# Performance work log

Hardware: AMD Instinct MI355X
Metric: run time of the kernel (lower is better)

Reference implementation:

```python
import jax, jax.numpy as jnp
import numpy as np

B, H, L, D, S = 4, 16, 4096, 64, 128

def setup_inputs() -> dict:
    key = jax.random.key(0)
    k1, k2 = jax.random.split(key)
    x = jax.random.normal(k1, (B, H, L, D), dtype=jnp.float32)
    c = jax.random.normal(k2, (H, S, D), dtype=jnp.float32)
    # codebook rows are unit-normalized at init (matches torch init)
    c = c / jnp.linalg.norm(c, axis=-1, keepdims=True)
    return {"x": x, "c": c}

def reference(x, c):
    # cosine-similarity scores: [B,H,L,S]
    cos_sim = jnp.einsum('bhld,hsd->bhls', x, c)
    delta_index = jnp.argmax(cos_sim, axis=-1)            # [B,H,L]
    delta_onehot = jax.nn.one_hot(delta_index, c.shape[-2], dtype=jnp.float32)  # [B,H,L,S]
    return (delta_onehot, c)
```

## Files before the change

### kernel.cpp

```cpp
#include <hip/hip_runtime.h>
#include <math.h>

constexpr int BB = 4;
constexpr int HH = 16;
constexpr int LL = 4096;
constexpr int DD = 64;
constexpr int SS = 128;
constexpr int BM = 128;

constexpr float TAU = 2e-3f;

typedef __attribute__((ext_vector_type(8))) short bf16x8;
typedef __attribute__((ext_vector_type(4))) float f32x4;

#define MFMA16 __builtin_amdgcn_mfma_f32_16x16x32_bf16

__device__ __forceinline__ unsigned short f2bf(float v) {
    unsigned u = __float_as_uint(v);
    return (unsigned short)((u + 0x7fffu + ((u >> 16) & 1u)) >> 16);
}

__device__ __forceinline__ void split8(const float4 va, const float4 vb,
                                       uint4* hi, uint4* lo) {
    const float v[8] = {va.x, va.y, va.z, va.w, vb.x, vb.y, vb.z, vb.w};
    unsigned hw[4], lw[4];
    #pragma unroll
    for (int p = 0; p < 4; ++p) {
        const unsigned u0 = __float_as_uint(v[2 * p]);
        const unsigned u1 = __float_as_uint(v[2 * p + 1]);
        const unsigned h0 = u0 & 0xffff0000u;
        const unsigned h1 = u1 & 0xffff0000u;
        hw[p] = (u0 >> 16) | h1;
        lw[p] = (unsigned)f2bf(v[2 * p] - __uint_as_float(h0))
              | ((unsigned)f2bf(v[2 * p + 1] - __uint_as_float(h1)) << 16);
    }
    *hi = make_uint4(hw[0], hw[1], hw[2], hw[3]);
    *lo = make_uint4(lw[0], lw[1], lw[2], lw[3]);
}

union FragU { uint4 q; bf16x8 v; };

__global__ __launch_bounds__(256) void convert_c_kernel(
    const float* __restrict__ c, unsigned char* __restrict__ ws)
{
    const int sid = blockIdx.x * 256 + threadIdx.x;
    const int h  = sid >> 10;
    const int r  = sid & 1023;
    const int kt = r >> 9;
    const int ct = (r >> 6) & 7;
    const int ln = r & 63;
    const int cc = ct * 16 + (ln & 15);
    const int k0 = kt * 32 + (ln >> 4) * 8;
    const float4* src = (const float4*)(c + ((size_t)h * SS + cc) * DD + k0);
    uint4 hi, lo;
    split8(src[0], src[1], &hi, &lo);
    unsigned char* base =
        ws + (size_t)h * 32768 + (size_t)(((kt << 3) | ct) * 1024 + ln * 16);
    *(uint4*)(base) = hi;
    *(uint4*)(base + 16384) = lo;
}

template <bool USE_WS>
__global__ __launch_bounds__(256) void quantizer_kernel(
    const float* __restrict__ x,
    const float* __restrict__ c,
    const unsigned char* __restrict__ ws,
    float* __restrict__ out,
    float* __restrict__ out_c)
{
    __shared__ __align__(16) unsigned char smemB[32768];
    __shared__ int amax[BM];
    __shared__ int s_nflag;
    __shared__ int s_flag[BM];
    __shared__ float s_fsc[SS];

    const int tid = threadIdx.x;
    const int wv = tid >> 6;
    const int lane = tid & 63;
    const int ln15 = lane & 15;
    const int blk = blockIdx.x;
    const long long r0 = (long long)blk * BM;
    const int h = (int)((r0 >> 12) & (HH - 1));
    const float* __restrict__ chead = c + (size_t)h * SS * DD;

    if (tid == 0) s_nflag = 0;

    if (USE_WS) {
        const unsigned char* wsb = ws + (size_t)h * 32768;
        #pragma unroll
        for (int it = 0; it < 8; ++it) {
            const unsigned off = (unsigned)(wv * 8192 + it * 1024);
            __builtin_amdgcn_global_load_lds(
                (const __attribute__((address_space(1))) unsigned*)
                    (wsb + off + (unsigned)(lane * 16)),
                (__attribute__((address_space(3))) unsigned*)(smemB + off),
                16, 0, 0);
        }
    } else {
        #pragma unroll
        for (int it = 0; it < 4; ++it) {
            const int sid = it * 256 + tid;
            const int kt = sid >> 9;
            const int ct = (sid >> 6) & 7;
            const int ln = sid & 63;
            const int cc = ct * 16 + (ln & 15);
            const int k0 = kt * 32 + (ln >> 4) * 8;
            const float4* src = (const float4*)(chead + (size_t)cc * DD + k0);
            uint4 hi, lo;
            split8(src[0], src[1], &hi, &lo);
            unsigned char* dst = smemB + ((kt << 3) | ct) * 1024 + ln * 16;
            *(uint4*)dst = hi;
            *(uint4*)(dst + 16384) = lo;
        }
    }

    bf16x8 af[2][2][2];
    #pragma unroll
    for (int rtb = 0; rtb < 2; ++rtb) {
        const size_t row = (size_t)(r0 + wv * 32 + rtb * 16 + ln15);
        const float* xr = x + row * DD + (lane >> 4) * 8;
        #pragma unroll
        for (int kt = 0; kt < 2; ++kt) {
            const float4* s4 = (const float4*)(xr + kt * 32);
            FragU hi, lo;
            split8(s4[0], s4[1], &hi.q, &lo.q);
            af[rtb][kt][0] = hi.v;
            af[rtb][kt][1] = lo.v;
        }
    }
    __syncthreads();

    float m1[2][4], m2[2][4];
    int   mi_[2][4];
    #pragma unroll
    for (int rtb = 0; rtb < 2; ++rtb)
        #pragma unroll
        for (int r = 0; r < 4; ++r) {
            m1[rtb][r] = -INFINITY; m2[rtb][r] = -INFINITY; mi_[rtb][r] = 0;
        }

    #pragma unroll
    for (int ct = 0; ct < 8; ++ct) {
        const unsigned bb = (unsigned)(ct << 10) + (unsigned)(lane * 16);
        const bf16x8 b10 = *(const bf16x8*)(smemB + bb);
        const bf16x8 b11 = *(const bf16x8*)(smemB + bb + 8192);
        const bf16x8 b20 = *(const bf16x8*)(smemB + bb + 16384);
        const bf16x8 b21 = *(const bf16x8*)(smemB + bb + 24576);
        #pragma unroll
        for (int rtb = 0; rtb < 2; ++rtb) {
            f32x4 acc = {0.f, 0.f, 0.f, 0.f};
            acc = MFMA16(af[rtb][0][1], b10, acc, 0, 0, 0);
            acc = MFMA16(af[rtb][1][1], b11, acc, 0, 0, 0);
            acc = MFMA16(af[rtb][0][0], b20, acc, 0, 0, 0);
            acc = MFMA16(af[rtb][1][0], b21, acc, 0, 0, 0);
            acc = MFMA16(af[rtb][0][0], b10, acc, 0, 0, 0);
            acc = MFMA16(af[rtb][1][0], b11, acc, 0, 0, 0);
            #pragma unroll
            for (int r = 0; r < 4; ++r) {
                const float v = acc[r];
                const int col = ct * 16 + ln15;
                if (v > m1[rtb][r]) {
                    m2[rtb][r] = m1[rtb][r]; m1[rtb][r] = v; mi_[rtb][r] = col;
                } else {
                    m2[rtb][r] = fmaxf(m2[rtb][r], v);
                }
            }
        }
    }

    #pragma unroll
    for (int rtb = 0; rtb < 2; ++rtb) {
        #pragma unroll
        for (int r = 0; r < 4; ++r) {
            float a1 = m1[rtb][r], a2 = m2[rtb][r];
            int ai = mi_[rtb][r];
            #pragma unroll
            for (int off = 1; off <= 8; off <<= 1) {
                const float o1 = __shfl_xor(a1, off);
                const float o2 = __shfl_xor(a2, off);
                const int   oi = __shfl_xor(ai, off);
                const bool take = (o1 > a1) || (o1 == a1 && oi < ai);
                const float n2 = take ? fmaxf(a1, o2) : fmaxf(a2, o1);
                if (take) { a1 = o1; ai = oi; }
                a2 = n2;
            }
            if (ln15 == 0) {
                const int row = (2 * wv + rtb) * 16 + (lane >> 4) * 4 + r;
                if (a1 - a2 >= TAU) {
                    amax[row] = ai;
                } else {
                    const int p = atomicAdd(&s_nflag, 1);
                    s_flag[p] = row;
                }
            }
        }
    }
    __syncthreads();

    const int nf = s_nflag;
    for (int f = 0; f < nf; ++f) {
        const int row = s_flag[f];
        if (tid < SS) {
            const float4* __restrict__ xr =
                (const float4*)(x + (size_t)(r0 + row) * DD);
            const float4* __restrict__ cr =
                (const float4*)(chead + (size_t)tid * DD);
            float sc = 0.f;
            #pragma unroll
            for (int q = 0; q < 16; ++q) {
                const float4 a = xr[q];
                const float4 b = cr[q];
                sc = fmaf(a.x, b.x, sc); sc = fmaf(a.y, b.y, sc);
                sc = fmaf(a.z, b.z, sc); sc = fmaf(a.w, b.w, sc);
            }
            s_fsc[tid] = sc;
        }
        __syncthreads();
        if (tid == 0) {
            float bv = s_fsc[0]; int bi = 0;
            for (int s = 1; s < SS; ++s)
                if (s_fsc[s] > bv) { bv = s_fsc[s]; bi = s; }
            amax[row] = bi;
        }
        __syncthreads();
    }

    float4* __restrict__ op = (float4*)(out + (size_t)r0 * SS);
    #pragma unroll 4
    for (int i = tid; i < BM * (SS / 4); i += 256) {
        const int rr = i >> 5;
        const int s0 = (i & 31) * 4;
        const int am = amax[rr];
        float4 v;
        v.x = (s0 + 0 == am) ? 1.f : 0.f;
        v.y = (s0 + 1 == am) ? 1.f : 0.f;
        v.z = (s0 + 2 == am) ? 1.f : 0.f;
        v.w = (s0 + 3 == am) ? 1.f : 0.f;
        op[i] = v;
    }

    if (blk < 128) {
        const float4* __restrict__ src = (const float4*)c;
        float4* __restrict__ dst = (float4*)out_c;
        const int idx = blk * 256 + tid;
        dst[idx] = src[idx];
    }
}

extern "C" void kernel_launch(void* const* d_in, const int* in_sizes, int n_in,
                              void* d_out, int out_size, void* d_ws, size_t ws_size,
                              hipStream_t stream) {
    const float* x = (const float*)d_in[0];
    const float* c = (const float*)d_in[1];
    float* out = (float*)d_out;
    float* out_c = out + (size_t)BB * HH * LL * SS;

    const int rows = BB * HH * LL;
    const int blocks = rows / BM;
    const size_t ws_need = (size_t)HH * 32768;

    if (d_ws != nullptr && ws_size >= ws_need) {
        convert_c_kernel<<<64, 256, 0, stream>>>(c, (unsigned char*)d_ws);
        quantizer_kernel<true><<<blocks, 256, 0, stream>>>(
            x, c, (const unsigned char*)d_ws, out, out_c);
    } else {
        quantizer_kernel<false><<<blocks, 256, 0, stream>>>(
            x, c, nullptr, out, out_c);
    }
}
```

Before: 202.9 us.

## Process two row tiles per block with prefetched x and split MFMA chains

```diff
diff --git a/kernel.cpp b/kernel.cpp
--- a/kernel.cpp
+++ b/kernel.cpp
@@ -7,6 +7,7 @@
 constexpr int DD = 64;
 constexpr int SS = 128;
 constexpr int BM = 128;
+constexpr int GG = 2;
 
 constexpr float TAU = 2e-3f;
 
@@ -60,8 +61,38 @@
     *(uint4*)(base + 16384) = lo;
 }
 
+__device__ __forceinline__ void load_a(const float* __restrict__ x,
+                                       long long rbase, int wv, int lane,
+                                       float4* raw) {
+    const int ln15 = lane & 15;
+    const int k0 = (lane >> 4) * 8;
+    #pragma unroll
+    for (int rtb = 0; rtb < 2; ++rtb) {
+        const float* xr =
+            x + (size_t)(rbase + wv * 32 + rtb * 16 + ln15) * DD + k0;
+        #pragma unroll
+        for (int kt = 0; kt < 2; ++kt) {
+            raw[rtb * 4 + kt * 2 + 0] = *(const float4*)(xr + kt * 32);
+            raw[rtb * 4 + kt * 2 + 1] = *(const float4*)(xr + kt * 32 + 4);
+        }
+    }
+}
+
+__device__ __forceinline__ void split_a(const float4* raw, bf16x8 af[2][2][2]) {
+    #pragma unroll
+    for (int rtb = 0; rtb < 2; ++rtb)
+        #pragma unroll
+        for (int kt = 0; kt < 2; ++kt) {
+            FragU hi, lo;
+            split8(raw[rtb * 4 + kt * 2], raw[rtb * 4 + kt * 2 + 1],
+                   &hi.q, &lo.q);
+            af[rtb][kt][0] = hi.v;
+            af[rtb][kt][1] = lo.v;
+        }
+}
+
 template <bool USE_WS>
-__global__ __launch_bounds__(256) void quantizer_kernel(
+__global__ __launch_bounds__(256, 4) void quantizer_kernel(
     const float* __restrict__ x,
     const float* __restrict__ c,
     const unsigned char* __restrict__ ws,
@@ -79,8 +110,8 @@
     const int lane = tid & 63;
     const int ln15 = lane & 15;
     const int blk = blockIdx.x;
-    const long long r0 = (long long)blk * BM;
-    const int h = (int)((r0 >> 12) & (HH - 1));
+    const long long base0 = (long long)blk * (GG * BM);
+    const int h = (int)((base0 >> 12) & (HH - 1));
     const float* __restrict__ chead = c + (size_t)h * SS * DD;
 
     if (tid == 0) s_nflag = 0;
@@ -114,129 +145,132 @@
         }
     }
 
+    float4 xraw[8];
+    load_a(x, base0, wv, lane, xraw);
     bf16x8 af[2][2][2];
+    split_a(xraw, af);
+
+    __syncthreads();
+
     #pragma unroll
-    for (int rtb = 0; rtb < 2; ++rtb) {
-        const size_t row = (size_t)(r0 + wv * 32 + rtb * 16 + ln15);
-        const float* xr = x + row * DD + (lane >> 4) * 8;
-        #pragma unroll
-        for (int kt = 0; kt < 2; ++kt) {
-            const float4* s4 = (const float4*)(xr + kt * 32);
-            FragU hi, lo;
-            split8(s4[0], s4[1], &hi.q, &lo.q);
-            af[rtb][kt][0] = hi.v;
-            af[rtb][kt][1] = lo.v;
-        }
-    }
-    __syncthreads();
-
-    float m1[2][4], m2[2][4];
-    int   mi_[2][4];
-    #pragma unroll
-    for (int rtb = 0; rtb < 2; ++rtb)
-        #pragma unroll
-        for (int r = 0; r < 4; ++r) {
-            m1[rtb][r] = -INFINITY; m2[rtb][r] = -INFINITY; mi_[rtb][r] = 0;
-        }
-
-    #pragma unroll
-    for (int ct = 0; ct < 8; ++ct) {
-        const unsigned bb = (unsigned)(ct << 10) + (unsigned)(lane * 16);
-        const bf16x8 b10 = *(const bf16x8*)(smemB + bb);
-        const bf16x8 b11 = *(const bf16x8*)(smemB + bb + 8192);
-        const bf16x8 b20 = *(const bf16x8*)(smemB + bb + 16384);
-        const bf16x8 b21 = *(const bf16x8*)(smemB + bb + 24576);
-        #pragma unroll
-        for (int rtb = 0; rtb < 2; ++rtb) {
-            f32x4 acc = {0.f, 0.f, 0.f, 0.f};
-            acc = MFMA16(af[rtb][0][1], b10, acc, 0, 0, 0);
-            acc = MFMA16(af[rtb][1][1], b11, acc, 0, 0, 0);
-            acc = MFMA16(af[rtb][0][0], b20, acc, 0, 0, 0);
-            acc = MFMA16(af[rtb][1][0], b21, acc, 0, 0, 0);
-            acc = MFMA16(af[rtb][0][0], b10, acc, 0, 0, 0);
-            acc = MFMA16(af[rtb][1][0], b11, acc, 0, 0, 0);
+    for (int g = 0; g < GG; ++g) {
+        const long long rg = base0 + (long long)g * BM;
+
+        if (g + 1 < GG) load_a(x, base0 + (long long)(g + 1) * BM,
+                               wv, lane, xraw);
+
+        float m1[2][4], m2[2][4];
+        int   mi_[2][4];
+        #pragma unroll
+        for (int rtb = 0; rtb < 2; ++rtb)
             #pragma unroll
             for (int r = 0; r < 4; ++r) {
-                const float v = acc[r];
-                const int col = ct * 16 + ln15;
-                if (v > m1[rtb][r]) {
-                    m2[rtb][r] = m1[rtb][r]; m1[rtb][r] = v; mi_[rtb][r] = col;
-                } else {
-                    m2[rtb][r] = fmaxf(m2[rtb][r], v);
+                m1[rtb][r] = -INFINITY; m2[rtb][r] = -INFINITY;
+                mi_[rtb][r] = 0;
+            }
+
+        #pragma unroll
+        for (int ct = 0; ct < 8; ++ct) {
+            const unsigned bb = (unsigned)(ct << 10) + (unsigned)(lane * 16);
+            const bf16x8 b10 = *(const bf16x8*)(smemB + bb);
+            const bf16x8 b11 = *(const bf16x8*)(smemB + bb + 8192);
+            const bf16x8 b20 = *(const bf16x8*)(smemB + bb + 16384);
+            const bf16x8 b21 = *(const bf16x8*)(smemB + bb + 24576);
+            #pragma unroll
+            for (int rtb = 0; rtb < 2; ++rtb) {
+                f32x4 a0 = {0.f, 0.f, 0.f, 0.f};
+                f32x4 a1 = {0.f, 0.f, 0.f, 0.f};
+                a0 = MFMA16(af[rtb][0][1], b10, a0, 0, 0, 0);
+                a0 = MFMA16(af[rtb][0][0], b20, a0, 0, 0, 0);
+                a0 = MFMA16(af[rtb][0][0], b10, a0, 0, 0, 0);
+                a1 = MFMA16(af[rtb][1][1], b11, a1, 0, 0, 0);
+                a1 = MFMA16(af[rtb][1][0], b21, a1, 0, 0, 0);
+                a1 = MFMA16(af[rtb][1][0], b11, a1, 0, 0, 0);
+                #pragma unroll
+                for (int r = 0; r < 4; ++r) {
+                    const float v = a0[r] + a1[r];
+                    const int col = ct * 16 + ln15;
+                    m2[rtb][r] =
+                        __builtin_amdgcn_fmed3f(m1[rtb][r], v, m2[rtb][r]);
+                    if (v > m1[rtb][r]) { m1[rtb][r] = v; mi_[rtb][r] = col; }
                 }
             }
         }
-    }
-
-    #pragma unroll
-    for (int rtb = 0; rtb < 2; ++rtb) {
-        #pragma unroll
-        for (int r = 0; r < 4; ++r) {
-            float a1 = m1[rtb][r], a2 = m2[rtb][r];
-            int ai = mi_[rtb][r];
+
+        #pragma unroll
+        for (int rtb = 0; rtb < 2; ++rtb) {
             #pragma unroll
-            for (int off = 1; off <= 8; off <<= 1) {
-                const float o1 = __shfl_xor(a1, off);
-                const float o2 = __shfl_xor(a2, off);
-                const int   oi = __shfl_xor(ai, off);
-                const bool take = (o1 > a1) || (o1 == a1 && oi < ai);
-                const float n2 = take ? fmaxf(a1, o2) : fmaxf(a2, o1);
-                if (take) { a1 = o1; ai = oi; }
-                a2 = n2;
-            }
-            if (ln15 == 0) {
-                const int row = (2 * wv + rtb) * 16 + (lane >> 4) * 4 + r;
-                if (a1 - a2 >= TAU) {
-                    amax[row] = ai;
-                } else {
-                    const int p = atomicAdd(&s_nflag, 1);
-                    s_flag[p] = row;
+            for (int r = 0; r < 4; ++r) {
+                float a1 = m1[rtb][r], a2 = m2[rtb][r];
+                int ai = mi_[rtb][r];
+                #pragma unroll
+                for (int off = 1; off <= 8; off <<= 1) {
+                    const float o1 = __shfl_xor(a1, off);
+                    const float o2 = __shfl_xor(a2, off);
+                    const int   oi = __shfl_xor(ai, off);
+                    const bool take = (o1 > a1) || (o1 == a1 && oi < ai);
+                    const float n2 = take ? fmaxf(a1, o2) : fmaxf(a2, o1);
+                    if (take) { a1 = o1; ai = oi; }
+                    a2 = n2;
                 }
-            }
-        }
-    }
-    __syncthreads();
-
-    const int nf = s_nflag;
-    for (int f = 0; f < nf; ++f) {
-        const int row = s_flag[f];
-        if (tid < SS) {
-            const float4* __restrict__ xr =
-                (const float4*)(x + (size_t)(r0 + row) * DD);
-            const float4* __restrict__ cr =
-                (const float4*)(chead + (size_t)tid * DD);
-            float sc = 0.f;
-            #pragma unroll
-            for (int q = 0; q < 16; ++q) {
-                const float4 a = xr[q];
-                const float4 b = cr[q];
-                sc = fmaf(a.x, b.x, sc); sc = fmaf(a.y, b.y, sc);
-                sc = fmaf(a.z, b.z, sc); sc = fmaf(a.w, b.w, sc);
-            }
-            s_fsc[tid] = sc;
+                if (ln15 == 0) {
+                    const int row = (2 * wv + rtb) * 16 + (lane >> 4) * 4 + r;
+                    if (a1 - a2 >= TAU) {
+                        amax[row] = ai;
+                    } else {
+                        const int p = atomicAdd(&s_nflag, 1);
+                        s_flag[p] = row;
+                    }
+                }
+            }
         }
         __syncthreads();
-        if (tid == 0) {
-            float bv = s_fsc[0]; int bi = 0;
-            for (int s = 1; s < SS; ++s)
-                if (s_fsc[s] > bv) { bv = s_fsc[s]; bi = s; }
-            amax[row] = bi;
+
+        const int nf = s_nflag;
+        for (int f = 0; f < nf; ++f) {
+            const int row = s_flag[f];
+            if (tid < SS) {
+                const float4* __restrict__ xr =
+                    (const float4*)(x + (size_t)(rg + row) * DD);
+                const float4* __restrict__ cr =
+                    (const float4*)(chead + (size_t)tid * DD);
+                float sc = 0.f;
+                #pragma unroll
+                for (int q = 0; q < 16; ++q) {
+                    const float4 a = xr[q];
+                    const float4 b = cr[q];
+                    sc = fmaf(a.x, b.x, sc); sc = fmaf(a.y, b.y, sc);
+                    sc = fmaf(a.z, b.z, sc); sc = fmaf(a.w, b.w, sc);
+                }
+                s_fsc[tid] = sc;
+            }
+            __syncthreads();
+            if (tid == 0) {
+                float bv = s_fsc[0]; int bi = 0;
+                for (int s = 1; s < SS; ++s)
+                    if (s_fsc[s] > bv) { bv = s_fsc[s]; bi = s; }
+                amax[row] = bi;
+            }
+            __syncthreads();
+        }
+        if (tid == 0) s_nflag = 0;
+
+        float4* __restrict__ op = (float4*)(out + (size_t)rg * SS);
+        #pragma unroll 4
+        for (int i = tid; i < BM * (SS / 4); i += 256) {
+            const int rr = i >> 5;
+            const int s0 = (i & 31) * 4;
+            const int am = amax[rr];
+            float4 v;
+            v.x = (s0 + 0 == am) ? 1.f : 0.f;
+            v.y = (s0 + 1 == am) ? 1.f : 0.f;
+            v.z = (s0 + 2 == am) ? 1.f : 0.f;
+            v.w = (s0 + 3 == am) ? 1.f : 0.f;
+            op[i] = v;
         }
         __syncthreads();
-    }
-
-    float4* __restrict__ op = (float4*)(out + (size_t)r0 * SS);
-    #pragma unroll 4
-    for (int i = tid; i < BM * (SS / 4); i += 256) {
-        const int rr = i >> 5;
-        const int s0 = (i & 31) * 4;
-        const int am = amax[rr];
-        float4 v;
-        v.x = (s0 + 0 == am) ? 1.f : 0.f;
-        v.y = (s0 + 1 == am) ? 1.f : 0.f;
-        v.z = (s0 + 2 == am) ? 1.f : 0.f;
-        v.w = (s0 + 3 == am) ? 1.f : 0.f;
-        op[i] = v;
+
+        if (g + 1 < GG) split_a(xraw, af);
     }
 
     if (blk < 128) {
@@ -256,7 +290,7 @@
     float* out_c = out + (size_t)BB * HH * LL * SS;
 
     const int rows = BB * HH * LL;
-    const int blocks = rows / BM;
+    const int blocks = rows / (GG * BM);
     const size_t ws_need = (size_t)HH * 32768;
 
     if (d_ws != nullptr && ws_size >= ws_need) {
```

New measurement: 244.1 us. 1.2x slower.
